# Kernel optimization log

Hardware: AMD Instinct MI355X
Metric: run time of the kernel (lower is better)

Reference implementation:

```python
import jax, jax.numpy as jnp
import numpy as np

FDIM = 512
H = W = 64
D_STATE = 16
D_INNER = 2 * FDIM
DT_RANK = FDIM // 16
K = 4


def conv2d(x, w, b=None, padding=0, dilation=1, groups=1):
    out = jax.lax.conv_general_dilated(
        x, w, (1, 1), [(padding, padding), (padding, padding)],
        rhs_dilation=(dilation, dilation), feature_group_count=groups,
        dimension_numbers=('NCHW', 'OIHW', 'NCHW'))
    if b is not None:
        out = out + b[None, :, None, None]
    return out


def layernorm(x, g, b, axes):
    mu = jnp.mean(x, axes, keepdims=True)
    var = jnp.var(x, axes, keepdims=True)
    return (x - mu) * jax.lax.rsqrt(var + 1e-5) * g + b


def channel_shuffle(x, groups):
    B, C, Hh, Ww = x.shape
    return x.reshape(B, groups, C // groups, Hh, Ww).transpose(0, 2, 1, 3, 4).reshape(B, C, Hh, Ww)


def selective_scan(u, delta, A, Bs, Cs, D):
    # u, delta: (B,K,d,L); A: (K,d,N); Bs, Cs: (B,K,N,L); D: (K,d)
    Bsz, Kk, d, L = u.shape
    N = A.shape[-1]
    dT = jnp.moveaxis(delta, -1, 0)  # (L,B,K,d)
    uT = jnp.moveaxis(u, -1, 0)
    BT = jnp.moveaxis(Bs, -1, 0)     # (L,B,K,N)
    CT = jnp.moveaxis(Cs, -1, 0)

    @jax.checkpoint
    def step(hprev, inp):
        dt, ut, bt, ct = inp
        dA = jnp.exp(dt[..., None] * A)                       # (B,K,d,N)
        hnew = dA * hprev + (dt * ut)[..., None] * bt[:, :, None, :]
        yt = jnp.einsum('bkdn,bkn->bkd', hnew, ct)
        return hnew, yt

    h0 = jnp.zeros((Bsz, Kk, d, N), u.dtype)
    _, ys = jax.lax.scan(step, h0, (dT, uT, BT, CT))          # ys: (L,B,K,d)
    y = jnp.moveaxis(ys, 0, -1)                               # (B,K,d,L)
    return y + D[None, :, :, None] * u


def ss2d_core(x, x_proj_w, dt_w, dt_b, A_logs, Ds):
    # x: (B, d_inner, H, W) -> y: (B, d_inner, L), VMamba 4-direction cross-scan
    B, d, Hh, Ww = x.shape
    L = Hh * Ww
    xf = x.reshape(B, d, L)
    xwh = jnp.swapaxes(x, 2, 3).reshape(B, d, L)
    x_hwwh = jnp.stack([xf, xwh], axis=1)                     # (B,2,d,L)
    xs = jnp.concatenate([x_hwwh, jnp.flip(x_hwwh, axis=-1)], axis=1)  # (B,4,d,L)
    x_dbl = jnp.einsum('bkdl,kcd->bkcl', xs, x_proj_w)
    dts, Bs, Cs = jnp.split(x_dbl, [DT_RANK, DT_RANK + D_STATE], axis=2)
    dts = jnp.einsum('bkrl,kdr->bkdl', dts, dt_w)
    delta = jax.nn.softplus(dts + dt_b[None, :, :, None])
    A = -jnp.exp(A_logs)
    out_y = selective_scan(xs, delta, A, Bs, Cs, Ds)          # (B,4,d,L)
    inv_y = jnp.flip(out_y[:, 2:4], axis=-1)
    wh_y = jnp.swapaxes(out_y[:, 1].reshape(B, d, Ww, Hh), 2, 3).reshape(B, d, L)
    invwh_y = jnp.swapaxes(inv_y[:, 1].reshape(B, d, Ww, Hh), 2, 3).reshape(B, d, L)
    return out_y[:, 0] + inv_y[:, 0] + wh_y + invwh_y


def setup_inputs() -> dict:
    key = jax.random.key(0)
    ks = jax.random.split(key, 16)
    rn = lambda k, shape, s=0.02: jax.random.normal(k, shape, jnp.float32) * s
    inp = {
        'feature_embedding': jax.random.normal(ks[0], (1, FDIM, H, W), jnp.float32),
        'latent_embedding': jax.random.normal(ks[1], (1, FDIM, H, W), jnp.float32),
        'fg_w1': rn(ks[2], (FDIM // 16, 2 * FDIM, 1, 1)),
        'fg_b1': jnp.zeros((FDIM // 16,), jnp.float32),
        'fg_w2': rn(ks[3], (2 * FDIM, FDIM // 16, 1, 1)),
        'fg_b2': jnp.zeros((2 * FDIM,), jnp.float32),
        'fb_w1': rn(ks[4], (FDIM, 2 * FDIM, 3, 3)),
        'ln_g': jnp.ones((FDIM, H, W), jnp.float32),
        'ln_b': jnp.zeros((FDIM, H, W), jnp.float32),
        'fb_dw_w': rn(ks[5], (FDIM, 1, 3, 3), 0.1),
        'fb_dw_b': jnp.zeros((FDIM,), jnp.float32),
        'fb_pw1_w': rn(ks[6], (FDIM, FDIM, 1, 1)),
        'fb_pw1_b': jnp.zeros((FDIM,), jnp.float32),
        'fb_pw2_w': rn(ks[7], (FDIM, FDIM, 1, 1)),
        'fb_pw2_b': jnp.zeros((FDIM,), jnp.float32),
        'ln1_g': jnp.ones((FDIM,), jnp.float32),
        'ln1_b': jnp.zeros((FDIM,), jnp.float32),
        'in_proj_w': rn(ks[8], (2 * D_INNER, FDIM)),
        'dconv_w': rn(ks[9], (D_INNER, 1, 3, 3), 0.1),
        'dconv_b': jnp.zeros((D_INNER,), jnp.float32),
        'x_proj_w': rn(ks[10], (K, DT_RANK + 2 * D_STATE, D_INNER)),
        'dt_w': rn(ks[11], (K, D_INNER, DT_RANK), 0.1),
        'dt_b': rn(ks[12], (K, D_INNER), 0.1) - 4.0,
        'A_logs': jnp.broadcast_to(jnp.log(jnp.arange(1, D_STATE + 1, dtype=jnp.float32)), (K, D_INNER, D_STATE)) + 0.0,
        'Ds': jnp.ones((K, D_INNER), jnp.float32),
        'out_norm_g': jnp.ones((D_INNER,), jnp.float32),
        'out_norm_b': jnp.zeros((D_INNER,), jnp.float32),
        'out_proj_w': rn(ks[13], (FDIM, D_INNER)),
    }
    return inp


def reference(feature_embedding, latent_embedding, fg_w1, fg_b1, fg_w2, fg_b2,
              fb_w1, ln_g, ln_b, fb_dw_w, fb_dw_b, fb_pw1_w, fb_pw1_b,
              fb_pw2_w, fb_pw2_b, ln1_g, ln1_b, in_proj_w, dconv_w, dconv_b,
              x_proj_w, dt_w, dt_b, A_logs, Ds, out_norm_g, out_norm_b, out_proj_w):
    gelu = lambda v: jax.nn.gelu(v, approximate=False)
    concat = jnp.concatenate([feature_embedding, latent_embedding], axis=1)
    g = gelu(conv2d(concat, fg_w1, fg_b1))
    g = jax.nn.sigmoid(conv2d(g, fg_w2, fg_b2))
    wf = concat * g
    h = conv2d(wf, fb_w1, padding=1)
    h = gelu(layernorm(h, ln_g, ln_b, (1, 2, 3)))
    h = conv2d(h, fb_dw_w, fb_dw_b, padding=2, dilation=2, groups=FDIM)
    h = gelu(conv2d(h, fb_pw1_w, fb_pw1_b))
    h = channel_shuffle(h, 8)
    h = conv2d(h, fb_pw2_w, fb_pw2_b)
    fused = h + feature_embedding                              # (B,C,H,W)
    B = fused.shape[0]
    # VSSBlock: LN -> SS2D -> residual, operating on (B,H,W,C)
    x = jnp.transpose(fused, (0, 2, 3, 1))
    xn = layernorm(x, ln1_g, ln1_b, (3,))
    xz = xn @ in_proj_w.T                                      # (B,H,W,2*d_inner)
    xp, z = jnp.split(xz, 2, axis=-1)
    xc = jnp.transpose(xp, (0, 3, 1, 2))                       # (B,d_inner,H,W)
    xc = jax.nn.silu(conv2d(xc, dconv_w, dconv_b, padding=1, groups=D_INNER))
    y = ss2d_core(xc, x_proj_w, dt_w, dt_b, A_logs, Ds)        # (B,d_inner,L)
    y = jnp.transpose(y.reshape(B, D_INNER, H, W), (0, 2, 3, 1))
    y = layernorm(y, out_norm_g, out_norm_b, (3,))
    y = y * jax.nn.silu(z)
    attn = x + (y @ out_proj_w.T)                              # VSSBlock residual
    attn_out = jnp.transpose(attn, (0, 3, 1, 2))               # (B,C,H,W)
    blur_k = jnp.full((FDIM, 1, 3, 3), 1.0 / 9.0, attn_out.dtype)  # AvgPool2d(3,1,1)
    return conv2d(attn_out, blur_k, padding=1, groups=FDIM) + fused
```

## Files before the change

### kernel.cpp

```cpp
#include <hip/hip_runtime.h>


#define NT 4096
#define NCH 32
#define CHL 128

__device__ __forceinline__ float geluf(float x){ return 0.5f*x*(1.f+erff(x*0.70710678118654752f)); }
__device__ __forceinline__ float sigmf(float x){ return 1.f/(1.f+__expf(-x)); }
__device__ __forceinline__ float softplusf(float x){ return (x>20.f)? x : __logf(1.f+__expf(x)); }
__device__ __forceinline__ unsigned short f2b(float f){
  unsigned u = __float_as_uint(f);
  u += 0x7FFFu + ((u>>16)&1u);
  return (unsigned short)(u>>16);
}

template<int BMODE, int EPI, bool TRANSW, int ZB=0>
__launch_bounds__(256)
__global__ void k_gemm(int M, int K, int lda, int ldb,
    const float* __restrict__ A, const float* __restrict__ bias,
    const float* __restrict__ Bf, const float* __restrict__ Bc0,
    const float* __restrict__ Bc1, int rev, int shuf,
    const float* __restrict__ resf, float* __restrict__ out)
{
  __shared__ float smem[4352];
  float* As = smem;
  float* Bs = smem + 2176;
  const int t  = threadIdx.x;
  const int n0 = blockIdx.x*64, m0 = blockIdx.y*64;
  if (ZB==1){
    int z = blockIdx.z;
    A   += (size_t)z*64*1024;
    if (z&1) Bf = Bc0;
    rev  = (z>=2);
    out += (size_t)z*NT*64;
  } else if (ZB==2){
    int z = blockIdx.z;
    A    += (size_t)z*1024*32;
    bias += (size_t)z*1024;
    Bf   += (size_t)z*NT*64;
    out  += (size_t)z*1024*NT;
  }
  float acc[4][4] = {};

  for (int k0=0; k0<K; k0+=32){
    __syncthreads();
    {
      int m = t>>2, kk0 = (t&3)*8;
      float av[8] = {0,0,0,0,0,0,0,0};
      if (m0+m < M){
        const float* pa = A + (size_t)(m0+m)*lda + k0 + kk0;
        float4 a0 = *(const float4*)pa; float4 a1 = *(const float4*)(pa+4);
        av[0]=a0.x; av[1]=a0.y; av[2]=a0.z; av[3]=a0.w;
        av[4]=a1.x; av[5]=a1.y; av[6]=a1.z; av[7]=a1.w;
      }
      #pragma unroll
      for (int j=0;j<8;j++) As[(kk0+j)*68 + m] = av[j];
    }
    if (BMODE==2){
      int n = t>>2, kk0 = (t&3)*8;
      const float* p = Bf + (size_t)(n0+n)*ldb + k0 + kk0;
      float4 x0 = *(const float4*)p; float4 x1 = *(const float4*)(p+4);
      Bs[(kk0+0)*68+n]=x0.x; Bs[(kk0+1)*68+n]=x0.y; Bs[(kk0+2)*68+n]=x0.z; Bs[(kk0+3)*68+n]=x0.w;
      Bs[(kk0+4)*68+n]=x1.x; Bs[(kk0+5)*68+n]=x1.y; Bs[(kk0+6)*68+n]=x1.z; Bs[(kk0+7)*68+n]=x1.w;
    } else {
      int kk = t>>3, n8 = (t&7)*8;
      float bv[8];
      if (BMODE==0){
        int r = k0+kk; if (shuf) r = (r&7)*64 + (r>>3);
        const float* p = Bf + (size_t)r*NT;
        if (!rev){
          float4 x0 = *(const float4*)(p + n0+n8); float4 x1 = *(const float4*)(p + n0+n8+4);
          bv[0]=x0.x;bv[1]=x0.y;bv[2]=x0.z;bv[3]=x0.w;bv[4]=x1.x;bv[5]=x1.y;bv[6]=x1.z;bv[7]=x1.w;
        } else {
          const float* q = p + (4088 - n0 - n8);
          float4 x0 = *(const float4*)q; float4 x1 = *(const float4*)(q+4);
          bv[0]=x1.w;bv[1]=x1.z;bv[2]=x1.y;bv[3]=x1.x;bv[4]=x0.w;bv[5]=x0.z;bv[6]=x0.y;bv[7]=x0.x;
        }
      } else if (BMODE==1){
        int c = k0+kk;
        const float* p = (c<512) ? (Bc0 + (size_t)c*NT) : (Bc1 + (size_t)(c-512)*NT);
        float4 x0 = *(const float4*)(p + n0+n8); float4 x1 = *(const float4*)(p + n0+n8+4);
        bv[0]=x0.x;bv[1]=x0.y;bv[2]=x0.z;bv[3]=x0.w;bv[4]=x1.x;bv[5]=x1.y;bv[6]=x1.z;bv[7]=x1.w;
      } else {
        #pragma unroll
        for (int j=0;j<8;j++) bv[j] = 0.f;
      }
      *(float4*)&Bs[kk*68 + n8]   = make_float4(bv[0],bv[1],bv[2],bv[3]);
      *(float4*)&Bs[kk*68 + n8+4] = make_float4(bv[4],bv[5],bv[6],bv[7]);
    }
    __syncthreads();
    int ti = t>>4, tj = t&15;
    #pragma unroll
    for (int kk=0; kk<32; kk++){
      float4 a4 = *(const float4*)&As[kk*68 + ti*4];
      float4 b4 = *(const float4*)&Bs[kk*68 + tj*4];
      float aa[4] = {a4.x,a4.y,a4.z,a4.w};
      float bb[4] = {b4.x,b4.y,b4.z,b4.w};
      #pragma unroll
      for (int i=0;i<4;i++)
        #pragma unroll
        for (int j=0;j<4;j++) acc[i][j] += aa[i]*bb[j];
    }
  }

  int ti = t>>4, tj = t&15;
  if (!TRANSW){
    #pragma unroll
    for (int i=0;i<4;i++){
      int m = m0 + ti*4 + i;
      if (m >= M) continue;
      float bi = bias ? bias[m] : 0.f;
      float o4[4];
      #pragma unroll
      for (int j=0;j<4;j++){
        int n = n0 + tj*4 + j;
        float v = acc[i][j] + bi;
        if (EPI==1) v = geluf(v);
        else if (EPI==2) v = softplusf(v);
        else if (EPI==4) v = v + resf[(size_t)m*NT + n];
        else if (EPI==5){
          float cv = (m<512)? Bc0[(size_t)m*NT+n] : Bc1[(size_t)(m-512)*NT+n];
          v = cv * sigmf(v);
        }
        o4[j] = v;
      }
      *(float4*)&out[(size_t)m*NT + n0 + tj*4] = make_float4(o4[0],o4[1],o4[2],o4[3]);
    }
  } else {
    __syncthreads();
    #pragma unroll
    for (int i=0;i<4;i++)
      #pragma unroll
      for (int j=0;j<4;j++)
        smem[(tj*4+j)*68 + (ti*4+i)] = acc[i][j];
    __syncthreads();
    int nl = t>>2, c0 = (t&3)*16;
    #pragma unroll
    for (int g4=0; g4<4; g4++){
      float4 v = *(const float4*)&smem[nl*68 + c0 + g4*4];
      *(float4*)&out[(size_t)(n0+nl)*64 + c0 + g4*4] = v;
    }
  }
}

__global__ void k_cvt_bf16(const float* __restrict__ in, unsigned short* __restrict__ outp){
  size_t i = ((size_t)blockIdx.x*256 + threadIdx.x)*8;
  float4 a = *(const float4*)(in+i), b = *(const float4*)(in+i+4);
  unsigned short o[8] = { f2b(a.x),f2b(a.y),f2b(a.z),f2b(a.w),
                          f2b(b.x),f2b(b.y),f2b(b.z),f2b(b.w) };
  *(int4*)(outp+i) = *(int4*)o;
}

__global__ void k_cvt_wfrag(const float* __restrict__ w, int lda, int KSn,
                            unsigned short* __restrict__ outp){
  int tid = blockIdx.x*256 + threadIdx.x;
  int lane = tid & 63;
  int tmp = tid >> 6;
  int KS = tmp % KSn, MT = tmp / KSn;
  int m = MT*16 + (lane&15);
  int k = KS*32 + (lane>>4)*8;
  const float* p = w + (size_t)m*lda + k;
  float4 a = *(const float4*)p, b = *(const float4*)(p+4);
  unsigned short o[8] = { f2b(a.x),f2b(a.y),f2b(a.z),f2b(a.w),
                          f2b(b.x),f2b(b.y),f2b(b.z),f2b(b.w) };
  *(int4*)(outp + (size_t)tid*8) = *(int4*)o;
}

typedef __attribute__((ext_vector_type(8))) short bf16x8;
typedef __attribute__((ext_vector_type(4))) float f32x4;

__launch_bounds__(256)
__global__ void k_conv_mfma(const unsigned short* __restrict__ Wf,
                            const unsigned short* __restrict__ Bb,
                            float* __restrict__ outp){
  __shared__ unsigned short Bs[128*40];
  int t = threadIdx.x;
  int n0 = blockIdx.x*128, m0y = blockIdx.y;
  int kz = blockIdx.z;
  int w = t>>6, lane = t&63;
  int wm = (w>>1)*64, wn = (w&1)*64;
  int ln15 = lane&15, lhi = lane>>4;
  f32x4 acc[4][4] = {};
  int sn = t & 127, kh = t>>7;
  int p = n0 + sn, py = p>>6, px = p&63;

  for (int ks=0; ks<36; ks++){
    unsigned short tmp[16];
    int kbase = kz*1152 + ks*32 + kh*16;
    #pragma unroll
    for (int j=0;j<16;j++){
      int ka = kbase + j;
      int c = ka/9; int t9 = ka - c*9; int qy = t9/3;
      int dy = qy-1, dx = t9 - qy*3 - 1;
      int yy = py+dy, xx = px+dx;
      tmp[j] = (yy>=0 && yy<64 && xx>=0 && xx<64) ? Bb[(size_t)c*4096 + yy*64 + xx]
                                                  : (unsigned short)0;
    }
    __syncthreads();
    *(int4*)&Bs[sn*40 + kh*16]     = *(int4*)&tmp[0];
    *(int4*)&Bs[sn*40 + kh*16 + 8] = *(int4*)&tmp[8];
    __syncthreads();
    bf16x8 af[4], bf[4];
    int KSab = kz*36 + ks;
    #pragma unroll
    for (int fm=0; fm<4; fm++){
      int MT = m0y*8 + (w>>1)*4 + fm;
      af[fm] = *(const bf16x8*)&Wf[((size_t)MT*288 + KSab)*512 + lane*8];
    }
    #pragma unroll
    for (int fn=0; fn<4; fn++)
      bf[fn] = *(const bf16x8*)&Bs[(wn + fn*16 + ln15)*40 + lhi*8];
    #pragma unroll
    for (int fm=0; fm<4; fm++)
      #pragma unroll
      for (int fn=0; fn<4; fn++)
        acc[fm][fn] = __builtin_amdgcn_mfma_f32_16x16x32_bf16(af[fm], bf[fn], acc[fm][fn], 0,0,0);
  }
  float* op = outp + (size_t)kz*512*4096;
  #pragma unroll
  for (int fm=0; fm<4; fm++){
    #pragma unroll
    for (int fn=0; fn<4; fn++){
      int col = n0 + wn + fn*16 + ln15;
      int rowb = m0y*128 + wm + fm*16 + lhi*4;
      #pragma unroll
      for (int r=0; r<4; r++)
        op[(size_t)(rowb+r)*4096 + col] = acc[fm][fn][r];
    }
  }
}

__launch_bounds__(256)
__global__ void k_xz_mfma(const unsigned short* __restrict__ Wf,
                          const unsigned short* __restrict__ xnb,
                          float* __restrict__ outp){
  __shared__ unsigned short Bs[128*40];
  int t = threadIdx.x;
  int n0 = blockIdx.x*128, m0y = blockIdx.y;
  int w = t>>6, lane = t&63;
  int wm = (w>>1)*64, wn = (w&1)*64;
  int ln15 = lane&15, lhi = lane>>4;
  f32x4 acc[4][4] = {};
  int sn = t & 127, kh = t>>7;

  for (int ks=0; ks<16; ks++){
    const unsigned short* src = xnb + (size_t)(n0+sn)*512 + ks*32 + kh*16;
    int4 v0 = *(const int4*)src;
    int4 v1 = *(const int4*)(src+8);
    __syncthreads();
    *(int4*)&Bs[sn*40 + kh*16]     = v0;
    *(int4*)&Bs[sn*40 + kh*16 + 8] = v1;
    __syncthreads();
    bf16x8 af[4], bf[4];
    #pragma unroll
    for (int fm=0; fm<4; fm++){
      int MT = m0y*8 + (w>>1)*4 + fm;
      af[fm] = *(const bf16x8*)&Wf[((size_t)MT*16 + ks)*512 + lane*8];
    }
    #pragma unroll
    for (int fn=0; fn<4; fn++)
      bf[fn] = *(const bf16x8*)&Bs[(wn + fn*16 + ln15)*40 + lhi*8];
    #pragma unroll
    for (int fm=0; fm<4; fm++)
      #pragma unroll
      for (int fn=0; fn<4; fn++)
        acc[fm][fn] = __builtin_amdgcn_mfma_f32_16x16x32_bf16(af[fm], bf[fn], acc[fm][fn], 0,0,0);
  }
  #pragma unroll
  for (int fm=0; fm<4; fm++){
    #pragma unroll
    for (int fn=0; fn<4; fn++){
      int col = n0 + wn + fn*16 + ln15;
      int rowb = m0y*128 + wm + fm*16 + lhi*4;
      #pragma unroll
      for (int r=0; r<4; r++)
        outp[(size_t)(rowb+r)*4096 + col] = acc[fm][fn][r];
    }
  }
}

template<int DIL, int ACT>
__global__ void k_dwconv(const float* __restrict__ in, const float* __restrict__ w,
                         const float* __restrict__ b, float* __restrict__ out){
  int bid = blockIdx.x;
  int c = bid >> 4, yb = bid & 15;
  int t = threadIdx.x;
  int y = yb*4 + (t>>6), x = t&63;
  const float* pin = in + (size_t)c*NT;
  float acc = b[c];
  #pragma unroll
  for (int ky=0; ky<3; ky++){
    int yy = y + DIL*(ky-1);
    if (yy<0 || yy>=64) continue;
    #pragma unroll
    for (int kx=0; kx<3; kx++){
      int xx = x + DIL*(kx-1);
      if (xx<0 || xx>=64) continue;
      acc += w[c*9 + ky*3 + kx] * pin[yy*64+xx];
    }
  }
  if (ACT==1) acc = acc * sigmf(acc);
  out[(size_t)c*NT + y*64 + x] = acc;
}

__global__ void k_red_part8(const float* __restrict__ hp, float* __restrict__ h,
                            float* __restrict__ part){
  __shared__ float ls[256], lq[256];
  int t = threadIdx.x; size_t base = (size_t)blockIdx.x*4096 + t;
  const size_t SL = (size_t)512*4096;
  float s=0, q=0;
  #pragma unroll
  for (int i=0;i<16;i++){
    size_t idx = base + i*256;
    float v = 0.f;
    #pragma unroll
    for (int z=0; z<8; z++) v += hp[idx + z*SL];
    h[idx] = v; s+=v; q+=v*v;
  }
  ls[t]=s; lq[t]=q; __syncthreads();
  for (int off=128; off; off>>=1){ if (t<off){ ls[t]+=ls[t+off]; lq[t]+=lq[t+off]; } __syncthreads(); }
  if (t==0){ part[blockIdx.x] = ls[0]; part[512 + blockIdx.x] = lq[0]; }
}
__global__ void k_red_fin(const float* __restrict__ part, float* __restrict__ stats){
  __shared__ float ls[256], lq[256];
  int t = threadIdx.x;
  ls[t] = part[t] + part[t+256];
  lq[t] = part[512+t] + part[768+t];
  __syncthreads();
  for (int off=128; off; off>>=1){ if (t<off){ ls[t]+=ls[t+off]; lq[t]+=lq[t+off]; } __syncthreads(); }
  if (t==0){
    float mu = ls[0] * (1.f/2097152.f);
    float var = lq[0]*(1.f/2097152.f) - mu*mu;
    stats[0]=mu; stats[1]=rsqrtf(var + 1e-5f);
  }
}
__global__ void k_ln_gelu(const float* __restrict__ h, const float* __restrict__ g,
                          const float* __restrict__ b, const float* __restrict__ stats,
                          float* __restrict__ out){
  size_t idx = ((size_t)blockIdx.x*256 + threadIdx.x)*4;
  float mu = stats[0], rs = stats[1];
  float4 hv = *(const float4*)(h + idx);
  float4 gv = *(const float4*)(g + idx);
  float4 bv = *(const float4*)(b + idx);
  float4 o;
  o.x = geluf((hv.x-mu)*rs*gv.x+bv.x);
  o.y = geluf((hv.y-mu)*rs*gv.y+bv.y);
  o.z = geluf((hv.z-mu)*rs*gv.z+bv.z);
  o.w = geluf((hv.w-mu)*rs*gv.w+bv.w);
  *(float4*)(out + idx) = o;
}

__global__ void k_ln1_stats(const float* __restrict__ fused, float* __restrict__ mu1,
                            float* __restrict__ rs1){
  __shared__ float ss[256], sq[256];
  int t = threadIdx.x; int ci = t>>6; int pj = t&63;
  int pos = blockIdx.x*64 + pj;
  float s=0,q=0;
  for (int c=ci; c<512; c+=4){ float v = fused[(size_t)c*NT + pos]; s+=v; q+=v*v; }
  ss[t]=s; sq[t]=q; __syncthreads();
  if (ci==0){
    float S = ss[pj]+ss[64+pj]+ss[128+pj]+ss[192+pj];
    float Q = sq[pj]+sq[64+pj]+sq[128+pj]+sq[192+pj];
    float mu = S*(1.f/512.f);
    mu1[pos]=mu; rs1[pos]=rsqrtf(Q*(1.f/512.f) - mu*mu + 1e-5f);
  }
}
__global__ void k_ln1_apply(const float* __restrict__ fused, const float* __restrict__ g,
                            const float* __restrict__ b, const float* __restrict__ mu1,
                            const float* __restrict__ rs1, unsigned short* __restrict__ xnb){
  __shared__ float tile[64*65];
  int t = threadIdx.x;
  int p0 = blockIdx.x*64, c0 = blockIdx.y*64;
  for (int it=0; it<16; it++){
    int idx = t + it*256; int yy = idx>>6, xx = idx&63;
    tile[yy*65+xx] = fused[(size_t)(c0+yy)*NT + p0+xx];
  }
  __syncthreads();
  for (int it=0; it<16; it++){
    int idx = t + it*256; int r = idx>>6, s = idx&63;
    float v = tile[s*65+r];
    int pos = p0+r, c = c0+s;
    xnb[(size_t)pos*512 + c] = f2b((v - mu1[pos])*rs1[pos]*g[c] + b[c]);
  }
}

__global__ void k_transpose64(const float* __restrict__ in, float* __restrict__ out){
  __shared__ float tile[64*65];
  int d = blockIdx.x; int t = threadIdx.x;
  const float* p = in + (size_t)d*NT; float* q = out + (size_t)d*NT;
  for (int it=0; it<16; it++){
    int idx = t+it*256; int yy = idx>>6, xx = idx&63;
    tile[yy*65+xx] = p[idx];
  }
  __syncthreads();
  for (int it=0; it<16; it++){
    int idx = t+it*256; int w = idx>>6, hh = idx&63;
    q[idx] = tile[hh*65+w];
  }
}

__global__ void k_zero(float* __restrict__ p){
  size_t i = ((size_t)blockIdx.x*256 + threadIdx.x)*4;
  *(float4*)(p+i) = make_float4(0,0,0,0);
}

__launch_bounds__(64)
__global__ void k_scan_part(const float* __restrict__ delta, const float* __restrict__ xc,
                            const float* __restrict__ xcT, const float* __restrict__ xdblT,
                            const float* __restrict__ A_logs,
                            float* __restrict__ Pbuf, float* __restrict__ Sbuf){
  int bid = blockIdx.x;
  int ss = bid / NCH;
  int c  = bid % NCH;
  int k = ss >> 6;
  int dbase = (ss & 63)*16;
  int lane = threadIdx.x;
  int dsub = lane & 15, ngrp = lane >> 4;
  int d = dbase + dsub;
  const float* up = ((k&1)? xcT : xc) + (size_t)d*NT;
  const float* dp = delta + ((size_t)(k*1024 + d))*NT;
  const float* bc = xdblT + (size_t)k*NT*64;
  float A[4], S[4]={0,0,0,0}, P[4]={1.f,1.f,1.f,1.f};
  #pragma unroll
  for (int j=0;j<4;j++) A[j] = -__expf(A_logs[(size_t)(k*1024+d)*16 + ngrp*4 + j]);
  const bool rv = (k>=2);
  int base = c*CHL;
  for (int l0=base; l0<base+CHL; l0+=4){
    float4 dv4 = *(const float4*)(dp + l0);
    float4 uraw = rv ? *(const float4*)(up + (4092-l0)) : *(const float4*)(up + l0);
    float dts[4] = {dv4.x,dv4.y,dv4.z,dv4.w};
    float us[4];
    if (rv){ us[0]=uraw.w; us[1]=uraw.z; us[2]=uraw.y; us[3]=uraw.x; }
    else   { us[0]=uraw.x; us[1]=uraw.y; us[2]=uraw.z; us[3]=uraw.w; }
    #pragma unroll
    for (int s=0;s<4;s++){
      int l = l0+s;
      float dt = dts[s];
      float4 B4 = *(const float4*)(bc + (size_t)l*64 + 32 + ngrp*4);
      float xbu = dt*us[s];
      float Bv[4]={B4.x,B4.y,B4.z,B4.w};
      #pragma unroll
      for (int j=0;j<4;j++){
        float dA = __expf(dt*A[j]);
        S[j] = dA*S[j] + xbu*Bv[j];
        P[j] *= dA;
      }
    }
  }
  size_t o = ((size_t)(k*1024+d)*NCH + c)*16 + ngrp*4;
  *(float4*)&Pbuf[o] = make_float4(P[0],P[1],P[2],P[3]);
  *(float4*)&Sbuf[o] = make_float4(S[0],S[1],S[2],S[3]);
}

__global__ void k_scan_comb(const float* __restrict__ Pbuf, const float* __restrict__ Sbuf,
                            float* __restrict__ Hbuf){
  int tid = blockIdx.x*256 + threadIdx.x;
  int scan = tid >> 4, n = tid & 15;
  size_t base = (size_t)scan*(NCH*16) + n;
  float h = 0.f;
  #pragma unroll
  for (int c=0;c<NCH;c++){
    Hbuf[base + c*16] = h;
    h = Pbuf[base + c*16]*h + Sbuf[base + c*16];
  }
}

__launch_bounds__(64)
__global__ void k_scan_fin(const float* __restrict__ delta, const float* __restrict__ xc,
                           const float* __restrict__ xcT, const float* __restrict__ xdblT,
                           const float* __restrict__ A_logs, const float* __restrict__ Ds,
                           const float* __restrict__ Hbuf, float* __restrict__ ycomb){
  int bid = blockIdx.x;
  int ss = bid / NCH;
  int c  = bid % NCH;
  int k = ss >> 6;
  int dbase = (ss & 63)*16;
  int lane = threadIdx.x;
  int dsub = lane & 15, ngrp = lane >> 4;
  int d = dbase + dsub;
  const float* up = ((k&1)? xcT : xc) + (size_t)d*NT;
  const float* dp = delta + ((size_t)(k*1024 + d))*NT;
  const float* bc = xdblT + (size_t)k*NT*64;
  float A[4], h[4];
  #pragma unroll
  for (int j=0;j<4;j++) A[j] = -__expf(A_logs[(size_t)(k*1024+d)*16 + ngrp*4 + j]);
  {
    size_t o = ((size_t)(k*1024+d)*NCH + c)*16 + ngrp*4;
    float4 h4 = *(const float4*)&Hbuf[o];
    h[0]=h4.x; h[1]=h4.y; h[2]=h4.z; h[3]=h4.w;
  }
  float Dv = Ds[k*1024+d];
  const bool rv = (k>=2);
  int base = c*CHL;
  for (int l0=base; l0<base+CHL; l0+=4){
    float4 dv4 = *(const float4*)(dp + l0);
    float4 uraw = rv ? *(const float4*)(up + (4092-l0)) : *(const float4*)(up + l0);
    float dts[4] = {dv4.x,dv4.y,dv4.z,dv4.w};
    float us[4];
    if (rv){ us[0]=uraw.w; us[1]=uraw.z; us[2]=uraw.y; us[3]=uraw.x; }
    else   { us[0]=uraw.x; us[1]=uraw.y; us[2]=uraw.z; us[3]=uraw.w; }
    #pragma unroll
    for (int s=0;s<4;s++){
      int l = l0+s;
      float dt = dts[s], u = us[s];
      float4 B4 = *(const float4*)(bc + (size_t)l*64 + 32 + ngrp*4);
      float4 C4 = *(const float4*)(bc + (size_t)l*64 + 48 + ngrp*4);
      float xbu = dt*u;
      float Bv[4]={B4.x,B4.y,B4.z,B4.w}, Cv[4]={C4.x,C4.y,C4.z,C4.w};
      float ys = 0.f;
      #pragma unroll
      for (int j=0;j<4;j++){
        float dA = __expf(dt*A[j]);
        h[j] = dA*h[j] + xbu*Bv[j];
        ys += h[j]*Cv[j];
      }
      ys += __shfl_xor(ys, 16);
      ys += __shfl_xor(ys, 32);
      if (ngrp==0){
        int pos;
        if (k==0) pos = l;
        else if (k==1) pos = ((l&63)<<6) | (l>>6);
        else if (k==2) pos = 4095-l;
        else { int tt = 4095-l; pos = ((tt&63)<<6) | (tt>>6); }
        atomicAdd(&ycomb[(size_t)pos*1024 + d], ys + Dv*u);
      }
    }
  }
}

__global__ void k_combine(const float* __restrict__ ycomb, const float* __restrict__ xz,
                          const float* __restrict__ g, const float* __restrict__ b,
                          float* __restrict__ yact){
  int pos = blockIdx.x, t = threadIdx.x;
  float v[4]; float s=0,q=0;
  #pragma unroll
  for (int i=0;i<4;i++){ v[i] = ycomb[(size_t)pos*1024 + t + i*256]; s+=v[i]; q+=v[i]*v[i]; }
  #pragma unroll
  for (int off=32; off>=1; off>>=1){ s += __shfl_xor(s,off); q += __shfl_xor(q,off); }
  __shared__ float red[8];
  int wid = t>>6;
  if ((t&63)==0){ red[wid*2]=s; red[wid*2+1]=q; }
  __syncthreads();
  float S = red[0]+red[2]+red[4]+red[6];
  float Q = red[1]+red[3]+red[5]+red[7];
  float mu = S*(1.f/1024.f), rs = rsqrtf(Q*(1.f/1024.f) - mu*mu + 1e-5f);
  #pragma unroll
  for (int i=0;i<4;i++){
    int dd = t + i*256;
    float z = xz[(size_t)(1024+dd)*NT + pos];
    float yv = (v[i]-mu)*rs*g[dd] + b[dd];
    yact[(size_t)pos*1024 + dd] = yv * (z * sigmf(z));
  }
}

__global__ void k_blur(const float* __restrict__ attn, const float* __restrict__ fused,
                       float* __restrict__ outp){
  int bid = blockIdx.x; int c = bid>>4, yb = bid&15; int t = threadIdx.x;
  int y = yb*4 + (t>>6), x = t&63;
  const float* p = attn + (size_t)c*NT;
  float s = 0;
  #pragma unroll
  for (int dy=-1; dy<=1; dy++){
    int yy = y+dy; if (yy<0||yy>=64) continue;
    #pragma unroll
    for (int dx=-1; dx<=1; dx++){
      int xx = x+dx; if (xx<0||xx>=64) continue;
      s += p[yy*64+xx];
    }
  }
  float val = s*(1.f/9.f) + fused[(size_t)c*NT + y*64 + x];
  outp[(size_t)c*NT + y*64 + x] = val;
}

extern "C" void kernel_launch(void* const* d_in, const int* in_sizes, int n_in,
                              void* d_out, int out_size, void* d_ws, size_t ws_size,
                              hipStream_t stream){
  const float* feat = (const float*)d_in[0];
  const float* lat  = (const float*)d_in[1];
  const float* fg_w1= (const float*)d_in[2];
  const float* fg_b1= (const float*)d_in[3];
  const float* fg_w2= (const float*)d_in[4];
  const float* fg_b2= (const float*)d_in[5];
  const float* fb_w1= (const float*)d_in[6];
  const float* ln_g = (const float*)d_in[7];
  const float* ln_b = (const float*)d_in[8];
  const float* dw_w = (const float*)d_in[9];
  const float* dw_b = (const float*)d_in[10];
  const float* pw1_w= (const float*)d_in[11];
  const float* pw1_b= (const float*)d_in[12];
  const float* pw2_w= (const float*)d_in[13];
  const float* pw2_b= (const float*)d_in[14];
  const float* ln1_g= (const float*)d_in[15];
  const float* ln1_b= (const float*)d_in[16];
  const float* inpw = (const float*)d_in[17];
  const float* dc_w = (const float*)d_in[18];
  const float* dc_b = (const float*)d_in[19];
  const float* xpw  = (const float*)d_in[20];
  const float* dtw  = (const float*)d_in[21];
  const float* dtb  = (const float*)d_in[22];
  const float* Alog = (const float*)d_in[23];
  const float* Dsp  = (const float*)d_in[24];
  const float* ong  = (const float*)d_in[25];
  const float* onb  = (const float*)d_in[26];
  const float* opw  = (const float*)d_in[27];
  float* outp = (float*)d_out;
  (void)in_sizes; (void)n_in; (void)out_size; (void)ws_size;

  float* Wp = (float*)d_ws;
  size_t off = 0;
  auto alloc = [&](size_t n){ float* p = Wp + off; off += n; return p; };
  float* S0    = alloc((size_t)1024*NT);
  float* S1    = alloc((size_t)512*NT);
  float* P0    = alloc((size_t)512*NT);
  float* P1    = alloc((size_t)2048*NT);
  float* P2    = alloc((size_t)1024*NT);
  float* P3    = alloc((size_t)1024*NT);
  float* P4    = alloc((size_t)4*NT*64);
  float* P5    = alloc((size_t)4*1024*NT);
  float* P6    = alloc((size_t)1024*NT);
  float* part  = alloc(1024);
  float* stats = alloc(4);
  float* mu1   = alloc(4096);
  float* rs1   = alloc(4096);

  float* wf    = S0;
  float* h     = S1;
  float* h2    = P1;
  float* h3    = S1;
  float* h4    = P2;
  float* fused = P0;
  float* xz    = P1;
  float* xc    = P2;
  float* xcT   = P3;
  float* xdblT = P4;
  float* hpart = P5;
  float* delta = P5;
  float* g1    = P6;
  float* ycomb = P6;
  float* yact  = S0;
  float* attn  = S1;
  unsigned short* wf_bf   = (unsigned short*)(P1 + (size_t)512*NT);
  unsigned short* w_frag  = (unsigned short*)(P1 + (size_t)1024*NT);
  unsigned short* xnb     = (unsigned short*)S0;
  unsigned short* w_frag2 = (unsigned short*)P5;
  float* Pbuf  = S0;
  float* Sbuf  = S0 + (size_t)2*1048576;
  float* Hbuf  = S1;

  hipLaunchKernelGGL((k_gemm<1,1,false>), dim3(64,1), dim3(256), 0, stream,
      32, 1024, 1024, 0, fg_w1, fg_b1, nullptr, feat, lat, 0,0, nullptr, g1);
  hipLaunchKernelGGL((k_gemm<0,5,false>), dim3(64,16), dim3(256), 0, stream,
      1024, 32, 32, 0, fg_w2, fg_b2, g1, feat, lat, 0,0, nullptr, wf);
  hipLaunchKernelGGL(k_cvt_bf16, dim3(2048), dim3(256), 0, stream, wf, wf_bf);
  hipLaunchKernelGGL(k_cvt_wfrag, dim3(2304), dim3(256), 0, stream, fb_w1, 9216, 288, w_frag);
  hipLaunchKernelGGL(k_conv_mfma, dim3(32,4,8), dim3(256), 0, stream, w_frag, wf_bf, hpart);
  hipLaunchKernelGGL(k_red_part8, dim3(512), dim3(256), 0, stream, hpart, h, part);
  hipLaunchKernelGGL(k_red_fin,  dim3(1),   dim3(256), 0, stream, part, stats);
  hipLaunchKernelGGL(k_ln_gelu,  dim3(2048),dim3(256), 0, stream, h, ln_g, ln_b, stats, h2);
  hipLaunchKernelGGL((k_dwconv<2,0>), dim3(512*16), dim3(256), 0, stream, h2, dw_w, dw_b, h3);
  hipLaunchKernelGGL((k_gemm<0,1,false>), dim3(64,8), dim3(256), 0, stream,
      512, 512, 512, 0, pw1_w, pw1_b, h3, nullptr,nullptr, 0,0, nullptr, h4);
  hipLaunchKernelGGL((k_gemm<0,4,false>), dim3(64,8), dim3(256), 0, stream,
      512, 512, 512, 0, pw2_w, pw2_b, h4, nullptr,nullptr, 0,1, feat, fused);
  hipLaunchKernelGGL(k_ln1_stats, dim3(64), dim3(256), 0, stream, fused, mu1, rs1);
  hipLaunchKernelGGL(k_ln1_apply, dim3(64,8), dim3(256), 0, stream, fused, ln1_g, ln1_b, mu1, rs1, xnb);
  hipLaunchKernelGGL(k_cvt_wfrag, dim3(512), dim3(256), 0, stream, inpw, 512, 16, w_frag2);
  hipLaunchKernelGGL(k_xz_mfma, dim3(32,16), dim3(256), 0, stream, w_frag2, xnb, xz);
  hipLaunchKernelGGL((k_dwconv<1,1>), dim3(1024*16), dim3(256), 0, stream, xz, dc_w, dc_b, xc);
  hipLaunchKernelGGL(k_transpose64, dim3(1024), dim3(256), 0, stream, xc, xcT);
  hipLaunchKernelGGL((k_gemm<0,0,true,1>), dim3(64,1,4), dim3(256), 0, stream,
      64, 1024, 1024, 0, xpw, nullptr, xc, xcT, nullptr, 0,0, nullptr, xdblT);
  hipLaunchKernelGGL((k_gemm<2,2,false,2>), dim3(64,16,4), dim3(256), 0, stream,
      1024, 32, 32, 64, dtw, dtb, xdblT, nullptr,nullptr, 0,0, nullptr, delta);
  hipLaunchKernelGGL(k_zero, dim3(4096), dim3(256), 0, stream, ycomb);
  hipLaunchKernelGGL(k_scan_part, dim3(256*NCH), dim3(64), 0, stream,
      delta, xc, xcT, xdblT, Alog, Pbuf, Sbuf);
  hipLaunchKernelGGL(k_scan_comb, dim3(256), dim3(256), 0, stream, Pbuf, Sbuf, Hbuf);
  hipLaunchKernelGGL(k_scan_fin, dim3(256*NCH), dim3(64), 0, stream,
      delta, xc, xcT, xdblT, Alog, Dsp, Hbuf, ycomb);
  hipLaunchKernelGGL(k_combine, dim3(4096), dim3(256), 0, stream, ycomb, xz, ong, onb, yact);
  hipLaunchKernelGGL((k_gemm<2,4,false>), dim3(64,8), dim3(256), 0, stream,
      512, 1024, 1024, 1024, opw, nullptr, yact, nullptr,nullptr, 0,0, fused, attn);
  hipLaunchKernelGGL(k_blur, dim3(512*16), dim3(256), 0, stream, attn, fused, outp);
}
```

Before: 1.080 ms.

## Run out_proj on bf16 MFMA and pack four scan warps per block

The xz MFMA kernel becomes a template over K-steps with an optional residual epilogue. It is then reused for the out_proj GEMM, which previously ran on the fp32 generic GEMM. k_combine now writes bf16 activations, and out_proj weights are converted to fragment layout each call. Separately, the scan part and fin kernels now place four 64-thread groups in one 256-thread block instead of one wave per block, cutting the block count. Running out_proj in bf16 lowers its precision.

Result: faster. 1.052 ms (-2.6%).

```diff
diff --git a/kernel.cpp b/kernel.cpp
--- a/kernel.cpp
+++ b/kernel.cpp
@@ -230,10 +230,12 @@
   }
 }
 
+template<int KSTEPS, int EPI>
 __launch_bounds__(256)
-__global__ void k_xz_mfma(const unsigned short* __restrict__ Wf,
-                          const unsigned short* __restrict__ xnb,
-                          float* __restrict__ outp){
+__global__ void k_nhwc_mfma(const unsigned short* __restrict__ Wf,
+                            const unsigned short* __restrict__ Bb, int ldb,
+                            const float* __restrict__ resf,
+                            float* __restrict__ outp){
   __shared__ unsigned short Bs[128*40];
   int t = threadIdx.x;
   int n0 = blockIdx.x*128, m0y = blockIdx.y;
@@ -243,8 +245,8 @@
   f32x4 acc[4][4] = {};
   int sn = t & 127, kh = t>>7;
 
-  for (int ks=0; ks<16; ks++){
-    const unsigned short* src = xnb + (size_t)(n0+sn)*512 + ks*32 + kh*16;
+  for (int ks=0; ks<KSTEPS; ks++){
+    const unsigned short* src = Bb + (size_t)(n0+sn)*ldb + ks*32 + kh*16;
     int4 v0 = *(const int4*)src;
     int4 v1 = *(const int4*)(src+8);
     __syncthreads();
@@ -255,7 +257,7 @@
     #pragma unroll
     for (int fm=0; fm<4; fm++){
       int MT = m0y*8 + (w>>1)*4 + fm;
-      af[fm] = *(const bf16x8*)&Wf[((size_t)MT*16 + ks)*512 + lane*8];
+      af[fm] = *(const bf16x8*)&Wf[((size_t)MT*KSTEPS + ks)*512 + lane*8];
     }
     #pragma unroll
     for (int fn=0; fn<4; fn++)
@@ -273,8 +275,11 @@
       int col = n0 + wn + fn*16 + ln15;
       int rowb = m0y*128 + wm + fm*16 + lhi*4;
       #pragma unroll
-      for (int r=0; r<4; r++)
-        outp[(size_t)(rowb+r)*4096 + col] = acc[fm][fn][r];
+      for (int r=0; r<4; r++){
+        float v = acc[fm][fn][r];
+        if (EPI==4) v += resf[(size_t)(rowb+r)*4096 + col];
+        outp[(size_t)(rowb+r)*4096 + col] = v;
+      }
     }
   }
 }
@@ -404,19 +409,20 @@
   *(float4*)(p+i) = make_float4(0,0,0,0);
 }
 
-__launch_bounds__(64)
+__launch_bounds__(256)
 __global__ void k_scan_part(const float* __restrict__ delta, const float* __restrict__ xc,
                             const float* __restrict__ xcT, const float* __restrict__ xdblT,
                             const float* __restrict__ A_logs,
                             float* __restrict__ Pbuf, float* __restrict__ Sbuf){
   int bid = blockIdx.x;
-  int ss = bid / NCH;
-  int c  = bid % NCH;
-  int k = ss >> 6;
-  int dbase = (ss & 63)*16;
-  int lane = threadIdx.x;
+  int c    = bid % NCH;
+  int rest = bid / NCH;
+  int k    = rest >> 4;
+  int dblk = rest & 15;
+  int w    = threadIdx.x >> 6;
+  int lane = threadIdx.x & 63;
   int dsub = lane & 15, ngrp = lane >> 4;
-  int d = dbase + dsub;
+  int d = dblk*64 + w*16 + dsub;
   const float* up = ((k&1)? xcT : xc) + (size_t)d*NT;
   const float* dp = delta + ((size_t)(k*1024 + d))*NT;
   const float* bc = xdblT + (size_t)k*NT*64;
@@ -465,19 +471,20 @@
   }
 }
 
-__launch_bounds__(64)
+__launch_bounds__(256)
 __global__ void k_scan_fin(const float* __restrict__ delta, const float* __restrict__ xc,
                            const float* __restrict__ xcT, const float* __restrict__ xdblT,
                            const float* __restrict__ A_logs, const float* __restrict__ Ds,
                            const float* __restrict__ Hbuf, float* __restrict__ ycomb){
   int bid = blockIdx.x;
-  int ss = bid / NCH;
-  int c  = bid % NCH;
-  int k = ss >> 6;
-  int dbase = (ss & 63)*16;
-  int lane = threadIdx.x;
+  int c    = bid % NCH;
+  int rest = bid / NCH;
+  int k    = rest >> 4;
+  int dblk = rest & 15;
+  int w    = threadIdx.x >> 6;
+  int lane = threadIdx.x & 63;
   int dsub = lane & 15, ngrp = lane >> 4;
-  int d = dbase + dsub;
+  int d = dblk*64 + w*16 + dsub;
   const float* up = ((k&1)? xcT : xc) + (size_t)d*NT;
   const float* dp = delta + ((size_t)(k*1024 + d))*NT;
   const float* bc = xdblT + (size_t)k*NT*64;
@@ -530,7 +537,7 @@
 
 __global__ void k_combine(const float* __restrict__ ycomb, const float* __restrict__ xz,
                           const float* __restrict__ g, const float* __restrict__ b,
-                          float* __restrict__ yact){
+                          unsigned short* __restrict__ yactb){
   int pos = blockIdx.x, t = threadIdx.x;
   float v[4]; float s=0,q=0;
   #pragma unroll
@@ -549,7 +556,7 @@
     int dd = t + i*256;
     float z = xz[(size_t)(1024+dd)*NT + pos];
     float yv = (v[i]-mu)*rs*g[dd] + b[dd];
-    yact[(size_t)pos*1024 + dd] = yv * (z * sigmf(z));
+    yactb[(size_t)pos*1024 + dd] = f2b(yv * (z * sigmf(z)));
   }
 }
 
@@ -637,12 +644,13 @@
   float* delta = P5;
   float* g1    = P6;
   float* ycomb = P6;
-  float* yact  = S0;
   float* attn  = S1;
   unsigned short* wf_bf   = (unsigned short*)(P1 + (size_t)512*NT);
   unsigned short* w_frag  = (unsigned short*)(P1 + (size_t)1024*NT);
   unsigned short* xnb     = (unsigned short*)S0;
   unsigned short* w_frag2 = (unsigned short*)P5;
+  unsigned short* yactb   = (unsigned short*)S0;
+  unsigned short* w_frag3 = (unsigned short*)P5;
   float* Pbuf  = S0;
   float* Sbuf  = S0 + (size_t)2*1048576;
   float* Hbuf  = S1;
@@ -665,7 +673,8 @@
   hipLaunchKernelGGL(k_ln1_stats, dim3(64), dim3(256), 0, stream, fused, mu1, rs1);
   hipLaunchKernelGGL(k_ln1_apply, dim3(64,8), dim3(256), 0, stream, fused, ln1_g, ln1_b, mu1, rs1, xnb);
   hipLaunchKernelGGL(k_cvt_wfrag, dim3(512), dim3(256), 0, stream, inpw, 512, 16, w_frag2);
-  hipLaunchKernelGGL(k_xz_mfma, dim3(32,16), dim3(256), 0, stream, w_frag2, xnb, xz);
+  hipLaunchKernelGGL((k_nhwc_mfma<16,0>), dim3(32,16), dim3(256), 0, stream,
+      w_frag2, xnb, 512, nullptr, xz);
   hipLaunchKernelGGL((k_dwconv<1,1>), dim3(1024*16), dim3(256), 0, stream, xz, dc_w, dc_b, xc);
   hipLaunchKernelGGL(k_transpose64, dim3(1024), dim3(256), 0, stream, xc, xcT);
   hipLaunchKernelGGL((k_gemm<0,0,true,1>), dim3(64,1,4), dim3(256), 0, stream,
@@ -673,13 +682,14 @@
   hipLaunchKernelGGL((k_gemm<2,2,false,2>), dim3(64,16,4), dim3(256), 0, stream,
       1024, 32, 32, 64, dtw, dtb, xdblT, nullptr,nullptr, 0,0, nullptr, delta);
   hipLaunchKernelGGL(k_zero, dim3(4096), dim3(256), 0, stream, ycomb);
-  hipLaunchKernelGGL(k_scan_part, dim3(256*NCH), dim3(64), 0, stream,
+  hipLaunchKernelGGL(k_scan_part, dim3(64*NCH), dim3(256), 0, stream,
       delta, xc, xcT, xdblT, Alog, Pbuf, Sbuf);
   hipLaunchKernelGGL(k_scan_comb, dim3(256), dim3(256), 0, stream, Pbuf, Sbuf, Hbuf);
-  hipLaunchKernelGGL(k_scan_fin, dim3(256*NCH), dim3(64), 0, stream,
+  hipLaunchKernelGGL(k_scan_fin, dim3(64*NCH), dim3(256), 0, stream,
       delta, xc, xcT, xdblT, Alog, Dsp, Hbuf, ycomb);
-  hipLaunchKernelGGL(k_combine, dim3(4096), dim3(256), 0, stream, ycomb, xz, ong, onb, yact);
-  hipLaunchKernelGGL((k_gemm<2,4,false>), dim3(64,8), dim3(256), 0, stream,
-      512, 1024, 1024, 1024, opw, nullptr, yact, nullptr,nullptr, 0,0, fused, attn);
+  hipLaunchKernelGGL(k_combine, dim3(4096), dim3(256), 0, stream, ycomb, xz, ong, onb, yactb);
+  hipLaunchKernelGGL(k_cvt_wfrag, dim3(256), dim3(256), 0, stream, opw, 1024, 32, w_frag3);
+  hipLaunchKernelGGL((k_nhwc_mfma<32,4>), dim3(32,4), dim3(256), 0, stream,
+      w_frag3, yactb, 1024, fused, attn);
   hipLaunchKernelGGL(k_blur, dim3(512*16), dim3(256), 0, stream, attn, fused, outp);
 }
```
